# Kernel optimization log

Hardware: AMD Instinct MI355X
Metric: run time of the kernel (lower is better)

The kernel has to match this reference:

```python
import jax, jax.numpy as jnp
import numpy as np


def lstm_scan(x, W, U, b, hidden):
    """Keras-style LSTM. x: [B,T,D]. Returns full hidden sequence [B,T,H].
    Gate order i,f,c,o; sigmoid recurrent activation, tanh cell activation."""
    B, T, D = x.shape
    H = hidden
    # Precompute input projections for all timesteps in one big GEMM: [B,T,4H]
    xz = jnp.einsum('btd,dk->btk', x, W) + b
    xz = jnp.transpose(xz, (1, 0, 2))  # [T,B,4H] for scan

    def step(carry, xz_t):
        h, c = carry
        z = xz_t + h @ U  # [B,4H]
        i = jax.nn.sigmoid(z[:, 0*H:1*H])
        f = jax.nn.sigmoid(z[:, 1*H:2*H])
        g = jnp.tanh(z[:, 2*H:3*H])
        o = jax.nn.sigmoid(z[:, 3*H:4*H])
        c_new = f * c + i * g
        h_new = o * jnp.tanh(c_new)
        return (h_new, c_new), h_new

    h0 = jnp.zeros((B, H), dtype=x.dtype)
    c0 = jnp.zeros((B, H), dtype=x.dtype)
    _, hs = jax.lax.scan(step, (h0, c0), xz)  # hs: [T,B,H]
    return jnp.transpose(hs, (1, 0, 2))  # [B,T,H]


def setup_inputs() -> dict:
    key = jax.random.key(0)
    ks = jax.random.split(key, 9)
    B, T, D = 512, 512, 300
    H1, H2, C = 128, 32, 14
    s = lambda fan: 1.0 / np.sqrt(fan)
    return {
        'x':  jax.random.normal(ks[0], (B, T, D), dtype=jnp.float32),
        'W1': jax.random.normal(ks[1], (D, 4 * H1), dtype=jnp.float32) * s(D),
        'U1': jax.random.normal(ks[2], (H1, 4 * H1), dtype=jnp.float32) * s(H1),
        'b1': jnp.zeros((4 * H1,), dtype=jnp.float32),
        'W2': jax.random.normal(ks[3], (H1, 4 * H2), dtype=jnp.float32) * s(H1),
        'U2': jax.random.normal(ks[4], (H2, 4 * H2), dtype=jnp.float32) * s(H2),
        'b2': jnp.zeros((4 * H2,), dtype=jnp.float32),
        'Wd': jax.random.normal(ks[5], (H2, C), dtype=jnp.float32) * s(H2),
        'bd': jnp.zeros((C,), dtype=jnp.float32),
    }


def reference(x, W1, U1, b1, W2, U2, b2, Wd, bd):
    h1 = lstm_scan(x, W1, U1, b1, 128)      # [B,T,128] (return_sequences=True)
    h2 = lstm_scan(h1, W2, U2, b2, 32)      # [B,T,32]
    h2_last = h2[:, -1, :]                  # return_sequences=False -> last step
    return jax.nn.softmax(h2_last @ Wd + bd, axis=-1)  # [B,14]
```

## Files before the change

### kernel.cpp

```cpp
#include <hip/hip_runtime.h>
#include <math.h>

#define TC 128
#define NC 4
#define BATCH 512
#define T_TOTAL 512
#define D_IN 300
#define KP1 320
#define H1 128
#define G1 512
#define H2 32
#define NCLS 14

typedef unsigned short u16;
typedef __attribute__((ext_vector_type(8))) _Float16 f16x8;
typedef __attribute__((ext_vector_type(4))) float f32x4;

__device__ __forceinline__ float fexp2(float x) { return __builtin_amdgcn_exp2f(x); }
__device__ __forceinline__ float frcp(float x)  { return __builtin_amdgcn_rcpf(x); }
__device__ __forceinline__ float sig_f(float x) { return frcp(1.0f + fexp2(-1.44269504f * x)); }
__device__ __forceinline__ float th_f(float x)  { return 1.0f - 2.0f * frcp(1.0f + fexp2(2.88539008f * x)); }

__device__ __forceinline__ void lds_barrier() {
    asm volatile("s_waitcnt lgkmcnt(0)" ::: "memory");
    __builtin_amdgcn_s_barrier();
}

__global__ void prep_weights(const float* __restrict__ U1, _Float16* __restrict__ U1p,
                             const float* __restrict__ U2, _Float16* __restrict__ U2p,
                             const float* __restrict__ W1, _Float16* __restrict__ W1T,
                             const float* __restrict__ W2, _Float16* __restrict__ W2T,
                             const float* __restrict__ b1, float* __restrict__ b1p,
                             const float* __restrict__ b2, float* __restrict__ b2p)
{
    int idx = blockIdx.x * 256 + threadIdx.x;
    if (idx < 512 * 128) {
        int p = idx >> 7, k = idx & 127;
        int orig = ((p >> 4) & 3) * 128 + ((p >> 6) << 4) + (p & 15);
        U1p[p * 128 + k] = (_Float16)U1[k * 512 + orig];
    }
    if (idx < 512 * 320) {
        int p = idx / 320, k = idx % 320;
        int orig = ((p >> 4) & 3) * 128 + ((p >> 6) << 4) + (p & 15);
        W1T[p * 320 + k] = (_Float16)((k < D_IN) ? W1[k * 512 + orig] : 0.f);
    }
    if (idx < 128 * 128) {
        int p = idx >> 7, k = idx & 127;
        int orig = ((p >> 4) & 3) * 32 + ((p >> 6) << 4) + (p & 15);
        W2T[p * 128 + k] = (_Float16)W2[k * 128 + orig];
    }
    if (idx < 128 * 32) {
        int p = idx >> 5, k = idx & 31;
        int orig = ((p >> 4) & 3) * 32 + ((p >> 6) << 4) + (p & 15);
        U2p[p * 32 + k] = (_Float16)U2[k * 128 + orig];
    }
    if (idx < 512) {
        int orig = ((idx >> 4) & 3) * 128 + ((idx >> 6) << 4) + (idx & 15);
        b1p[idx] = b1[orig];
    }
    if (idx < 128) {
        int orig = ((idx >> 4) & 3) * 32 + ((idx >> 6) << 4) + (idx & 15);
        b2p[idx] = b2[orig];
    }
}

__global__ void xsplit(const float* __restrict__ x, _Float16* __restrict__ xh)
{
    long gid = (long)blockIdx.x * 256 + threadIdx.x;
    if (gid >= 262144L * 40) return;
    int m  = (int)(gid / 40);
    int s  = (int)(gid % 40);
    int k0 = s * 8;
    const float* xr = x + (long)m * D_IN + k0;
    float4 v0 = {0.f, 0.f, 0.f, 0.f}, v1 = {0.f, 0.f, 0.f, 0.f};
    if (s < 37) {
        v0 = *(const float4*)(xr);
        v1 = *(const float4*)(xr + 4);
    } else if (s == 37) {
        v0 = *(const float4*)(xr);
    }
    f16x8 o;
    o[0] = (_Float16)v0.x; o[1] = (_Float16)v0.y;
    o[2] = (_Float16)v0.z; o[3] = (_Float16)v0.w;
    o[4] = (_Float16)v1.x; o[5] = (_Float16)v1.y;
    o[6] = (_Float16)v1.z; o[7] = (_Float16)v1.w;
    *(f16x8*)(xh + (long)m * KP1 + k0) = o;
}

template<int NK, int NT, bool XMAP>
__device__ __forceinline__ void gemm_mblock(
    const _Float16* __restrict__ A, const _Float16* __restrict__ B,
    const float* __restrict__ bias, float* __restrict__ C,
    int m0, int chunk)
{
    const int Nc = NT * 128;
    const int tid = threadIdx.x;
    const int l = tid & 63, w = tid >> 6;
    const int wm = w >> 2, wn = w & 3;
    const int lr = l & 15, q = l >> 4;
    const int koff = q * 8;
    const int LDA = NK * 32;

    const _Float16* ap[4];
#pragma unroll
    for (int fi = 0; fi < 4; fi++) {
        int m = m0 + wm * 64 + fi * 16 + lr;
        long row = XMAP ? ((long)(m >> 7) * T_TOTAL + (long)chunk * TC + (m & (TC - 1)))
                        : (long)m;
        ap[fi] = A + row * LDA + koff;
    }
    const _Float16* bp[NT * 2];
    float bv[NT * 2];
#pragma unroll
    for (int fj = 0; fj < NT * 2; fj++) {
        int col = (fj >> 1) * 128 + wn * 32 + (fj & 1) * 16 + lr;
        bp[fj] = B + (long)col * LDA + koff;
        bv[fj] = bias[col];
    }

    f32x4 acc[4][NT * 2];
#pragma unroll
    for (int fi = 0; fi < 4; fi++)
#pragma unroll
        for (int fj = 0; fj < NT * 2; fj++)
            acc[fi][fj] = (f32x4){bv[fj], bv[fj], bv[fj], bv[fj]};

    f16x8 acur[4], anxt[4];
#pragma unroll
    for (int fi = 0; fi < 4; fi++)
        acur[fi] = *(const f16x8*)(ap[fi]);

#pragma unroll
    for (int ks = 0; ks < NK; ks++) {
        f16x8 bb[NT * 2];
#pragma unroll
        for (int fj = 0; fj < NT * 2; fj++)
            bb[fj] = *(const f16x8*)(bp[fj] + ks * 32);
        if (ks + 1 < NK) {
#pragma unroll
            for (int fi = 0; fi < 4; fi++)
                anxt[fi] = *(const f16x8*)(ap[fi] + (ks + 1) * 32);
        }
#pragma unroll
        for (int fi = 0; fi < 4; fi++)
#pragma unroll
            for (int fj = 0; fj < NT * 2; fj++)
                acc[fi][fj] = __builtin_amdgcn_mfma_f32_16x16x32_f16(acur[fi], bb[fj], acc[fi][fj], 0, 0, 0);
#pragma unroll
        for (int fi = 0; fi < 4; fi++)
            acur[fi] = anxt[fi];
    }

#pragma unroll
    for (int fi = 0; fi < 4; fi++) {
        int mrow = m0 + wm * 64 + fi * 16 + q * 4;
#pragma unroll
        for (int fj = 0; fj < NT * 2; fj++) {
            int col = (fj >> 1) * 128 + wn * 32 + (fj & 1) * 16 + lr;
#pragma unroll
            for (int rr = 0; rr < 4; rr++)
                C[(long)(mrow + rr) * Nc + col] = acc[fi][fj][rr];
        }
    }
}

#define L1_DECL(P) float P##00, P##01, P##02, P##03, P##10, P##11, P##12, P##13, \
                         P##20, P##21, P##22, P##23, P##30, P##31, P##32, P##33;

#define L1_LOAD(P, T)                                                             \
    P##00 = xz[xr0 + (long)(T) * 512 +  0]; P##01 = xz[xr1 + (long)(T) * 512 +  0]; \
    P##02 = xz[xr2 + (long)(T) * 512 +  0]; P##03 = xz[xr3 + (long)(T) * 512 +  0]; \
    P##10 = xz[xr0 + (long)(T) * 512 + 16]; P##11 = xz[xr1 + (long)(T) * 512 + 16]; \
    P##12 = xz[xr2 + (long)(T) * 512 + 16]; P##13 = xz[xr3 + (long)(T) * 512 + 16]; \
    P##20 = xz[xr0 + (long)(T) * 512 + 32]; P##21 = xz[xr1 + (long)(T) * 512 + 32]; \
    P##22 = xz[xr2 + (long)(T) * 512 + 32]; P##23 = xz[xr3 + (long)(T) * 512 + 32]; \
    P##30 = xz[xr0 + (long)(T) * 512 + 48]; P##31 = xz[xr1 + (long)(T) * 512 + 48]; \
    P##32 = xz[xr2 + (long)(T) * 512 + 48]; P##33 = xz[xr3 + (long)(T) * 512 + 48];

#define L1_STEP(T, PB, XC, XN)                                                    \
{                                                                                 \
    f16x8 ah0 = *(const f16x8*)&Ah[(PB) * 2048 + lr * 128 + (((q     ) ^ lr) << 3)]; \
    f16x8 ah1 = *(const f16x8*)&Ah[(PB) * 2048 + lr * 128 + (((q +  4) ^ lr) << 3)]; \
    f16x8 ah2 = *(const f16x8*)&Ah[(PB) * 2048 + lr * 128 + (((q +  8) ^ lr) << 3)]; \
    f16x8 ah3 = *(const f16x8*)&Ah[(PB) * 2048 + lr * 128 + (((q + 12) ^ lr) << 3)]; \
    if (valid && (T) + 1 < TC) { L1_LOAD(XN, (T) + 1) }                           \
    f32x4 a0 = (f32x4){XC##00, XC##01, XC##02, XC##03};                           \
    f32x4 a1 = (f32x4){XC##10, XC##11, XC##12, XC##13};                           \
    f32x4 a2 = (f32x4){XC##20, XC##21, XC##22, XC##23};                           \
    f32x4 a3 = (f32x4){XC##30, XC##31, XC##32, XC##33};                           \
    a0 = __builtin_amdgcn_mfma_f32_16x16x32_f16(ah0, uh00, a0, 0, 0, 0);          \
    a1 = __builtin_amdgcn_mfma_f32_16x16x32_f16(ah0, uh10, a1, 0, 0, 0);          \
    a2 = __builtin_amdgcn_mfma_f32_16x16x32_f16(ah0, uh20, a2, 0, 0, 0);          \
    a3 = __builtin_amdgcn_mfma_f32_16x16x32_f16(ah0, uh30, a3, 0, 0, 0);          \
    a0 = __builtin_amdgcn_mfma_f32_16x16x32_f16(ah1, uh01, a0, 0, 0, 0);          \
    a1 = __builtin_amdgcn_mfma_f32_16x16x32_f16(ah1, uh11, a1, 0, 0, 0);          \
    a2 = __builtin_amdgcn_mfma_f32_16x16x32_f16(ah1, uh21, a2, 0, 0, 0);          \
    a3 = __builtin_amdgcn_mfma_f32_16x16x32_f16(ah1, uh31, a3, 0, 0, 0);          \
    a0 = __builtin_amdgcn_mfma_f32_16x16x32_f16(ah2, uh02, a0, 0, 0, 0);          \
    a1 = __builtin_amdgcn_mfma_f32_16x16x32_f16(ah2, uh12, a1, 0, 0, 0);          \
    a2 = __builtin_amdgcn_mfma_f32_16x16x32_f16(ah2, uh22, a2, 0, 0, 0);          \
    a3 = __builtin_amdgcn_mfma_f32_16x16x32_f16(ah2, uh32, a3, 0, 0, 0);          \
    a0 = __builtin_amdgcn_mfma_f32_16x16x32_f16(ah3, uh03, a0, 0, 0, 0);          \
    a1 = __builtin_amdgcn_mfma_f32_16x16x32_f16(ah3, uh13, a1, 0, 0, 0);          \
    a2 = __builtin_amdgcn_mfma_f32_16x16x32_f16(ah3, uh23, a2, 0, 0, 0);          \
    a3 = __builtin_amdgcn_mfma_f32_16x16x32_f16(ah3, uh33, a3, 0, 0, 0);          \
    float e0 = __shfl_xor(a0[2], 32, 64), g0 = __shfl_xor(a0[3], 32, 64);         \
    float e1 = __shfl_xor(a1[2], 32, 64), g1 = __shfl_xor(a1[3], 32, 64);         \
    float e2 = __shfl_xor(a2[2], 32, 64), g2 = __shfl_xor(a2[3], 32, 64);         \
    float e3 = __shfl_xor(a3[2], 32, 64), g3 = __shfl_xor(a3[3], 32, 64);         \
    float zA0 = hi ? e0 : a0[0], zA1 = hi ? e1 : a1[0];                           \
    float zA2 = hi ? e2 : a2[0], zA3 = hi ? e3 : a3[0];                           \
    float zB0 = hi ? g0 : a0[1], zB1 = hi ? g1 : a1[1];                           \
    float zB2 = hi ? g2 : a2[1], zB3 = hi ? g3 : a3[1];                           \
    {                                                                             \
        float iv = sig_f(zA0), fv = sig_f(zA1), gv = th_f(zA2), ov = sig_f(zA3);  \
        cstA = fv * cstA + iv * gv;                                               \
        float hv = ov * th_f(cstA);                                               \
        _Float16 hh = (_Float16)hv;                                               \
        Ah[((PB) ^ 1) * 2048 + rwA * 128 + idxA] = hh;                            \
        h1f[((long)(b0 + rwA) * TC + (T)) * 128 + cn] = hh;                       \
        if ((T) == TC - 1) {                                                      \
            s1h[(long)(b0 + rwA) * 128 + cn] = hv;                                \
            s1c[(long)(b0 + rwA) * 128 + cn] = cstA;                              \
        }                                                                         \
    }                                                                             \
    {                                                                             \
        float iv = sig_f(zB0), fv = sig_f(zB1), gv = th_f(zB2), ov = sig_f(zB3);  \
        cstB = fv * cstB + iv * gv;                                               \
        float hv = ov * th_f(cstB);                                               \
        _Float16 hh = (_Float16)hv;                                               \
        Ah[((PB) ^ 1) * 2048 + rwB * 128 + idxB] = hh;                            \
        h1f[((long)(b0 + rwB) * TC + (T)) * 128 + cn] = hh;                       \
        if ((T) == TC - 1) {                                                      \
            s1h[(long)(b0 + rwB) * 128 + cn] = hv;                                \
            s1c[(long)(b0 + rwB) * 128 + cn] = cstB;                              \
        }                                                                         \
    }                                                                             \
    lds_barrier();                                                                \
}

static __device__ __forceinline__ void lstm1_role(
    const float* __restrict__ xz, const _Float16* __restrict__ U1p,
    _Float16* __restrict__ h1f, float* __restrict__ s1h, float* __restrict__ s1c,
    int first, char* smc)
{
    const int tid = threadIdx.x;
    const int l = tid & 63, w = tid >> 6;
    const int lr = l & 15, q = l >> 4;
    const int koff = q * 8;
    const int cn = w * 16 + lr;
    const int b0 = blockIdx.x * 8;
    const int p0 = w * 64 + lr;
    const int bq = b0 + q * 4;
    const bool valid = (q < 2);
    const bool hi = (q >= 2);
    const int rwA = (q & 1) * 4 + (q >> 1) * 2;
    const int rwB = rwA + 1;
    const int idxA = (((cn >> 3) ^ rwA) << 3) + (cn & 7);
    const int idxB = (((cn >> 3) ^ rwB) << 3) + (cn & 7);

    _Float16* Ah = (_Float16*)smc;

    const long xr0 = ((long)(bq + 0) * TC) * 512 + p0;
    const long xr1 = ((long)(bq + 1) * TC) * 512 + p0;
    const long xr2 = ((long)(bq + 2) * TC) * 512 + p0;
    const long xr3 = ((long)(bq + 3) * TC) * 512 + p0;

    const _Float16* ub = U1p + (long)(w * 64 + lr) * 128 + koff;
    f16x8 uh00 = *(const f16x8*)(ub +    0 * 128 +  0);
    f16x8 uh01 = *(const f16x8*)(ub +    0 * 128 + 32);
    f16x8 uh02 = *(const f16x8*)(ub +    0 * 128 + 64);
    f16x8 uh03 = *(const f16x8*)(ub +    0 * 128 + 96);
    f16x8 uh10 = *(const f16x8*)(ub +   16 * 128 +  0);
    f16x8 uh11 = *(const f16x8*)(ub +   16 * 128 + 32);
    f16x8 uh12 = *(const f16x8*)(ub +   16 * 128 + 64);
    f16x8 uh13 = *(const f16x8*)(ub +   16 * 128 + 96);
    f16x8 uh20 = *(const f16x8*)(ub +   32 * 128 +  0);
    f16x8 uh21 = *(const f16x8*)(ub +   32 * 128 + 32);
    f16x8 uh22 = *(const f16x8*)(ub +   32 * 128 + 64);
    f16x8 uh23 = *(const f16x8*)(ub +   32 * 128 + 96);
    f16x8 uh30 = *(const f16x8*)(ub +   48 * 128 +  0);
    f16x8 uh31 = *(const f16x8*)(ub +   48 * 128 + 32);
    f16x8 uh32 = *(const f16x8*)(ub +   48 * 128 + 64);
    f16x8 uh33 = *(const f16x8*)(ub +   48 * 128 + 96);

#pragma unroll
    for (int r = 0; r < 4; r++) {
        int rw = q * 4 + r;
        float h = 0.f;
        if (valid && !first) h = s1h[(long)(b0 + rw) * 128 + cn];
        int idx = (((cn >> 3) ^ rw) << 3) + (cn & 7);
        Ah[rw * 128 + idx] = valid ? (_Float16)h : (_Float16)0.f;
        if (!valid) Ah[2048 + rw * 128 + idx] = (_Float16)0.f;
    }
    float cstA = 0.f, cstB = 0.f;
    if (!first) {
        cstA = s1c[(long)(b0 + rwA) * 128 + cn];
        cstB = s1c[(long)(b0 + rwB) * 128 + cn];
    }
    lds_barrier();

    L1_DECL(xa) L1_DECL(xb)
    if (valid) { L1_LOAD(xa, 0) }

    for (int t = 0; t < TC; t += 2) {
        L1_STEP(t,     0, xa, xb)
        L1_STEP(t + 1, 1, xb, xa)
    }
}

#define L2_LOAD(P, T)                                                             \
    P##00 = xz2[yr0 + (long)(T) * 128 +  0]; P##01 = xz2[yr1 + (long)(T) * 128 +  0]; \
    P##02 = xz2[yr2 + (long)(T) * 128 +  0]; P##03 = xz2[yr3 + (long)(T) * 128 +  0]; \
    P##10 = xz2[yr0 + (long)(T) * 128 + 16]; P##11 = xz2[yr1 + (long)(T) * 128 + 16]; \
    P##12 = xz2[yr2 + (long)(T) * 128 + 16]; P##13 = xz2[yr3 + (long)(T) * 128 + 16]; \
    P##20 = xz2[yr0 + (long)(T) * 128 + 32]; P##21 = xz2[yr1 + (long)(T) * 128 + 32]; \
    P##22 = xz2[yr2 + (long)(T) * 128 + 32]; P##23 = xz2[yr3 + (long)(T) * 128 + 32]; \
    P##30 = xz2[yr0 + (long)(T) * 128 + 48]; P##31 = xz2[yr1 + (long)(T) * 128 + 48]; \
    P##32 = xz2[yr2 + (long)(T) * 128 + 48]; P##33 = xz2[yr3 + (long)(T) * 128 + 48];

#define L2_STEP(T, PB, XC, XN)                                                    \
{                                                                                 \
    if (act) {                                                                    \
        f16x8 ah = *(const f16x8*)&Ah[(PB) * 640 + lr * 40 + koff];               \
        if ((T) + 1 < TC) { L2_LOAD(XN, (T) + 1) }                                \
        f32x4 a0 = (f32x4){XC##00, XC##01, XC##02, XC##03};                       \
        f32x4 a1 = (f32x4){XC##10, XC##11, XC##12, XC##13};                       \
        f32x4 a2 = (f32x4){XC##20, XC##21, XC##22, XC##23};                       \
        f32x4 a3 = (f32x4){XC##30, XC##31, XC##32, XC##33};                       \
        a0 = __builtin_amdgcn_mfma_f32_16x16x32_f16(ah, uh0, a0, 0, 0, 0);        \
        a1 = __builtin_amdgcn_mfma_f32_16x16x32_f16(ah, uh1, a1, 0, 0, 0);        \
        a2 = __builtin_amdgcn_mfma_f32_16x16x32_f16(ah, uh2, a2, 0, 0, 0);        \
        a3 = __builtin_amdgcn_mfma_f32_16x16x32_f16(ah, uh3, a3, 0, 0, 0);        \
        _Pragma("unroll")                                                         \
        for (int r = 0; r < 4; r++) {                                             \
            float iv = sig_f(a0[r]);                                              \
            float fv = sig_f(a1[r]);                                              \
            float gv = th_f(a2[r]);                                               \
            float ov = sig_f(a3[r]);                                              \
            float cc = (r == 0) ? cst0 : (r == 1) ? cst1 : (r == 2) ? cst2 : cst3;\
            cc = fv * cc + iv * gv;                                               \
            float hv = ov * th_f(cc);                                             \
            if (r == 0) cst0 = cc; else if (r == 1) cst1 = cc;                    \
            else if (r == 2) cst2 = cc; else cst3 = cc;                           \
            int rw = (q << 2) + r;                                                \
            Ah[((PB) ^ 1) * 640 + rw * 40 + cn] = (_Float16)hv;                   \
            if ((T) == TC - 1) {                                                  \
                s2h[(long)(b0 + rw) * 32 + cn] = hv;                              \
                s2c[(long)(b0 + rw) * 32 + cn] = cc;                              \
            }                                                                     \
        }                                                                         \
    }                                                                             \
    lds_barrier();                                                                \
}

static __device__ __forceinline__ void lstm2_role(
    const float* __restrict__ xz2, const _Float16* __restrict__ U2p,
    float* __restrict__ s2h, float* __restrict__ s2c, int first, char* smc)
{
    const int tid = threadIdx.x;
    const int b0 = (blockIdx.x - 64) * 16;
    const bool act = tid < 128;
    const int l = tid & 63, w = (tid >> 6) & 1;
    const int lr = l & 15, q = l >> 4;
    const int koff = q * 8;
    const int cn = w * 16 + lr;
    const int p0 = w * 64 + lr;
    const int bq = b0 + q * 4;

    const long yr0 = ((long)(bq + 0) * TC) * 128 + p0;
    const long yr1 = ((long)(bq + 1) * TC) * 128 + p0;
    const long yr2 = ((long)(bq + 2) * TC) * 128 + p0;
    const long yr3 = ((long)(bq + 3) * TC) * 128 + p0;

    _Float16* Ah = (_Float16*)smc;

    f16x8 uh0 = {}, uh1 = {}, uh2 = {}, uh3 = {};
    float cst0 = 0.f, cst1 = 0.f, cst2 = 0.f, cst3 = 0.f;
    L1_DECL(xa) L1_DECL(xb)

    if (act) {
        const _Float16* ub = U2p + (long)(w * 64 + lr) * 32 + koff;
        uh0 = *(const f16x8*)(ub +  0 * 32);
        uh1 = *(const f16x8*)(ub + 16 * 32);
        uh2 = *(const f16x8*)(ub + 32 * 32);
        uh3 = *(const f16x8*)(ub + 48 * 32);
#pragma unroll
        for (int r = 0; r < 4; r++) {
            int rw = q * 4 + r;
            float h = 0.f, c = 0.f;
            if (!first) {
                h = s2h[(long)(b0 + rw) * 32 + cn];
                c = s2c[(long)(b0 + rw) * 32 + cn];
            }
            if (r == 0) cst0 = c; else if (r == 1) cst1 = c;
            else if (r == 2) cst2 = c; else cst3 = c;
            Ah[rw * 40 + cn] = (_Float16)h;
        }
        L2_LOAD(xa, 0)
    }
    lds_barrier();

    for (int t = 0; t < TC; t += 2) {
        L2_STEP(t,     0, xa, xb)
        L2_STEP(t + 1, 1, xb, xa)
    }
}

__global__ void
__attribute__((amdgpu_flat_work_group_size(512, 512)))
__attribute__((amdgpu_waves_per_eu(2, 2)))
mega(
    const _Float16* __restrict__ xh,
    const _Float16* __restrict__ W1T, const float* __restrict__ b1p,
    const _Float16* __restrict__ W2T, const float* __restrict__ b2p,
    const _Float16* __restrict__ U1p, const _Float16* __restrict__ U2p,
    float* xz1_0, float* xz1_1, float* xz2_0, float* xz2_1,
    _Float16* h1f_0, _Float16* h1f_1,
    float* s1h, float* s1c, float* s2h, float* s2c,
    int cA, int cB, int g1, int g2)
{
    __shared__ __align__(16) char sm[8192];
    int bid = blockIdx.x;

    if (cA >= 0 && bid < 64) {
        const float* xz = (cA & 1) ? xz1_1 : xz1_0;
        _Float16* hf = (cA & 1) ? h1f_1 : h1f_0;
        lstm1_role(xz, U1p, hf, s1h, s1c, cA == 0, sm);
        return;
    }
    if (cB >= 0 && bid >= 64 && bid < 96) {
        const float* xz2 = (cB & 1) ? xz2_1 : xz2_0;
        lstm2_role(xz2, U2p, s2h, s2c, cB == 0, sm);
        return;
    }
    int cwid = bid, ncw = 256;
    if (cA >= 0) { ncw -= 64; cwid -= 64; }
    if (cB >= 0) { ncw -= 32; if (bid >= 96) cwid -= 32; }
    int ng1 = (g1 >= 0) ? (BATCH * TC / 128) : 0;
    int ng2 = (g2 >= 0) ? (BATCH * TC / 128) : 0;
    float* xz1o = (g1 >= 0 && (g1 & 1)) ? xz1_1 : xz1_0;
    float* xz2o = (g2 >= 0 && (g2 & 1)) ? xz2_1 : xz2_0;
    const _Float16* hf = (g2 >= 0 && (g2 & 1)) ? h1f_1 : h1f_0;
    for (int it = cwid; it < ng1 + ng2; it += ncw) {
        if (it < ng1)
            gemm_mblock<10, 4, true>(xh, W1T, b1p, xz1o, it * 128, g1);
        else
            gemm_mblock<4, 1, false>(hf, W2T, b2p, xz2o, (it - ng1) * 128, 0);
    }
}

__global__ __launch_bounds__(256)
void head_kernel(const float* __restrict__ h2, const float* __restrict__ Wd,
                 const float* __restrict__ bd, float* __restrict__ out)
{
    int b = blockIdx.x * 256 + threadIdx.x;
    float h[H2];
#pragma unroll
    for (int k = 0; k < H2; k += 4)
        *(float4*)&h[k] = *(const float4*)&h2[b * H2 + k];

    float lg[NCLS];
#pragma unroll
    for (int c = 0; c < NCLS; c++) lg[c] = bd[c];
#pragma unroll
    for (int k = 0; k < H2; k++) {
        float hv = h[k];
#pragma unroll
        for (int c = 0; c < NCLS; c++)
            lg[c] += hv * Wd[k * NCLS + c];
    }
    float m = lg[0];
#pragma unroll
    for (int c = 1; c < NCLS; c++) m = fmaxf(m, lg[c]);
    float s = 0.f;
#pragma unroll
    for (int c = 0; c < NCLS; c++) { lg[c] = __expf(lg[c] - m); s += lg[c]; }
    float inv = __fdividef(1.0f, s);
#pragma unroll
    for (int c = 0; c < NCLS; c++) out[b * NCLS + c] = lg[c] * inv;
}

extern "C" void kernel_launch(void* const* d_in, const int* in_sizes, int n_in,
                              void* d_out, int out_size, void* d_ws, size_t ws_size,
                              hipStream_t stream)
{
    const float* x  = (const float*)d_in[0];
    const float* W1 = (const float*)d_in[1];
    const float* U1 = (const float*)d_in[2];
    const float* b1 = (const float*)d_in[3];
    const float* W2 = (const float*)d_in[4];
    const float* U2 = (const float*)d_in[5];
    const float* b2 = (const float*)d_in[6];
    const float* Wd = (const float*)d_in[7];
    const float* bd = (const float*)d_in[8];
    float* out = (float*)d_out;

    char* ws = (char*)d_ws;
    float* xz1[2]    = {(float*)(ws + 0L),         (float*)(ws + 134217728L)};
    _Float16* xh     = (_Float16*)(ws + 268435456L);
    _Float16* h1f[2] = {(_Float16*)(ws + 436207616L), (_Float16*)(ws + 452984832L)};
    float* xz2[2]    = {(float*)(ws + 469762048L), (float*)(ws + 503316480L)};
    float* s1h       = (float*)(ws + 536870912L);
    float* s1c       = (float*)(ws + 537133056L);
    float* s2h       = (float*)(ws + 537395200L);
    float* s2c       = (float*)(ws + 537460736L);
    _Float16* U1p    = (_Float16*)(ws + 537526272L);
    _Float16* U2p    = (_Float16*)(ws + 537657344L);
    _Float16* W1T    = (_Float16*)(ws + 537665536L);
    _Float16* W2T    = (_Float16*)(ws + 537993216L);
    float* b1p       = (float*)(ws + 538025984L);
    float* b2p       = (float*)(ws + 538028032L);

    prep_weights<<<640, 256, 0, stream>>>(U1, U1p, U2, U2p, W1, W1T, W2, W2T,
                                          b1, b1p, b2, b2p);
    xsplit<<<40960, 256, 0, stream>>>(x, xh);

#define MEGA(cA_, cB_, g1_, g2_) \
    mega<<<256, 512, 0, stream>>>(xh, W1T, b1p, W2T, b2p, U1p, U2p, \
        xz1[0], xz1[1], xz2[0], xz2[1], h1f[0], h1f[1], \
        s1h, s1c, s2h, s2c, cA_, cB_, g1_, g2_)

    MEGA(-1, -1, 0, -1);
    for (int c = 0; c < NC; c++)
        MEGA(c, (c >= 2) ? c - 2 : -1, (c + 1 < NC) ? c + 1 : -1, (c >= 1) ? c - 1 : -1);
    MEGA(-1, NC - 2, -1, NC - 1);
    MEGA(-1, NC - 1, -1, -1);
#undef MEGA

    head_kernel<<<2, 256, 0, stream>>>(s2h, Wd, bd, out);
}
```

Measured before the change: 966.4 us.

## Chunk fp16 input conversion into mega launches and split MFMA accumulator chains

The standalone full-tensor fp32-to-fp16 conversion of x is split per time chunk. Only chunk 0 is converted up front, and chunks 1-3 are converted by the GEMM worker blocks inside the first two mega launches, so the conversion overlaps the LSTM recurrence blocks. Separately, the layer-1 recurrent step splits each gate's 4-deep dependent MFMA chain into two independent accumulators that are summed afterward, shortening the serial latency per timestep. The accumulator split costs extra registers and vector adds, and the fused conversion lengthens the worker portion of the first launches.

```diff
diff --git a/kernel.cpp b/kernel.cpp
--- a/kernel.cpp
+++ b/kernel.cpp
@@ -64,14 +64,15 @@
     }
 }
 
-__global__ void xsplit(const float* __restrict__ x, _Float16* __restrict__ xh)
-{
-    long gid = (long)blockIdx.x * 256 + threadIdx.x;
-    if (gid >= 262144L * 40) return;
-    int m  = (int)(gid / 40);
-    int s  = (int)(gid % 40);
+__device__ __forceinline__ void xsplit_item(const float* __restrict__ x,
+                                            _Float16* __restrict__ xh,
+                                            int chunk, long i)
+{
+    int rr = (int)(i / 40), s = (int)(i % 40);
+    int b = rr >> 7, tt = rr & 127;
+    long m = (long)b * T_TOTAL + (long)chunk * TC + tt;
     int k0 = s * 8;
-    const float* xr = x + (long)m * D_IN + k0;
+    const float* xr = x + m * D_IN + k0;
     float4 v0 = {0.f, 0.f, 0.f, 0.f}, v1 = {0.f, 0.f, 0.f, 0.f};
     if (s < 37) {
         v0 = *(const float4*)(xr);
@@ -84,7 +85,23 @@
     o[2] = (_Float16)v0.z; o[3] = (_Float16)v0.w;
     o[4] = (_Float16)v1.x; o[5] = (_Float16)v1.y;
     o[6] = (_Float16)v1.z; o[7] = (_Float16)v1.w;
-    *(f16x8*)(xh + (long)m * KP1 + k0) = o;
+    *(f16x8*)(xh + m * KP1 + k0) = o;
+}
+
+__global__ void xsplit_chunk(const float* __restrict__ x, _Float16* __restrict__ xh, int chunk)
+{
+    long gid = (long)blockIdx.x * 256 + threadIdx.x;
+    if (gid >= 65536L * 40) return;
+    xsplit_item(x, xh, chunk, gid);
+}
+
+__device__ __forceinline__ void xsplit_role(const float* __restrict__ x,
+                                            _Float16* __restrict__ xh,
+                                            int chunk, int cwid, int ncw)
+{
+    const int tid = threadIdx.x;
+    for (long i = (long)cwid * 512 + tid; i < 65536L * 40; i += (long)ncw * 512)
+        xsplit_item(x, xh, chunk, i);
 }
 
 template<int NK, int NT, bool XMAP>
@@ -184,26 +201,29 @@
     f16x8 ah2 = *(const f16x8*)&Ah[(PB) * 2048 + lr * 128 + (((q +  8) ^ lr) << 3)]; \
     f16x8 ah3 = *(const f16x8*)&Ah[(PB) * 2048 + lr * 128 + (((q + 12) ^ lr) << 3)]; \
     if (valid && (T) + 1 < TC) { L1_LOAD(XN, (T) + 1) }                           \
-    f32x4 a0 = (f32x4){XC##00, XC##01, XC##02, XC##03};                           \
-    f32x4 a1 = (f32x4){XC##10, XC##11, XC##12, XC##13};                           \
-    f32x4 a2 = (f32x4){XC##20, XC##21, XC##22, XC##23};                           \
-    f32x4 a3 = (f32x4){XC##30, XC##31, XC##32, XC##33};                           \
-    a0 = __builtin_amdgcn_mfma_f32_16x16x32_f16(ah0, uh00, a0, 0, 0, 0);          \
-    a1 = __builtin_amdgcn_mfma_f32_16x16x32_f16(ah0, uh10, a1, 0, 0, 0);          \
-    a2 = __builtin_amdgcn_mfma_f32_16x16x32_f16(ah0, uh20, a2, 0, 0, 0);          \
-    a3 = __builtin_amdgcn_mfma_f32_16x16x32_f16(ah0, uh30, a3, 0, 0, 0);          \
-    a0 = __builtin_amdgcn_mfma_f32_16x16x32_f16(ah1, uh01, a0, 0, 0, 0);          \
-    a1 = __builtin_amdgcn_mfma_f32_16x16x32_f16(ah1, uh11, a1, 0, 0, 0);          \
-    a2 = __builtin_amdgcn_mfma_f32_16x16x32_f16(ah1, uh21, a2, 0, 0, 0);          \
-    a3 = __builtin_amdgcn_mfma_f32_16x16x32_f16(ah1, uh31, a3, 0, 0, 0);          \
-    a0 = __builtin_amdgcn_mfma_f32_16x16x32_f16(ah2, uh02, a0, 0, 0, 0);          \
-    a1 = __builtin_amdgcn_mfma_f32_16x16x32_f16(ah2, uh12, a1, 0, 0, 0);          \
-    a2 = __builtin_amdgcn_mfma_f32_16x16x32_f16(ah2, uh22, a2, 0, 0, 0);          \
-    a3 = __builtin_amdgcn_mfma_f32_16x16x32_f16(ah2, uh32, a3, 0, 0, 0);          \
-    a0 = __builtin_amdgcn_mfma_f32_16x16x32_f16(ah3, uh03, a0, 0, 0, 0);          \
-    a1 = __builtin_amdgcn_mfma_f32_16x16x32_f16(ah3, uh13, a1, 0, 0, 0);          \
-    a2 = __builtin_amdgcn_mfma_f32_16x16x32_f16(ah3, uh23, a2, 0, 0, 0);          \
-    a3 = __builtin_amdgcn_mfma_f32_16x16x32_f16(ah3, uh33, a3, 0, 0, 0);          \
+    f32x4 a0a = (f32x4){XC##00, XC##01, XC##02, XC##03};                          \
+    f32x4 a1a = (f32x4){XC##10, XC##11, XC##12, XC##13};                          \
+    f32x4 a2a = (f32x4){XC##20, XC##21, XC##22, XC##23};                          \
+    f32x4 a3a = (f32x4){XC##30, XC##31, XC##32, XC##33};                          \
+    f32x4 a0b = (f32x4){0.f, 0.f, 0.f, 0.f};                                      \
+    f32x4 a1b = a0b, a2b = a0b, a3b = a0b;                                        \
+    a0a = __builtin_amdgcn_mfma_f32_16x16x32_f16(ah0, uh00, a0a, 0, 0, 0);        \
+    a1a = __builtin_amdgcn_mfma_f32_16x16x32_f16(ah0, uh10, a1a, 0, 0, 0);        \
+    a2a = __builtin_amdgcn_mfma_f32_16x16x32_f16(ah0, uh20, a2a, 0, 0, 0);        \
+    a3a = __builtin_amdgcn_mfma_f32_16x16x32_f16(ah0, uh30, a3a, 0, 0, 0);        \
+    a0b = __builtin_amdgcn_mfma_f32_16x16x32_f16(ah1, uh01, a0b, 0, 0, 0);        \
+    a1b = __builtin_amdgcn_mfma_f32_16x16x32_f16(ah1, uh11, a1b, 0, 0, 0);        \
+    a2b = __builtin_amdgcn_mfma_f32_16x16x32_f16(ah1, uh21, a2b, 0, 0, 0);        \
+    a3b = __builtin_amdgcn_mfma_f32_16x16x32_f16(ah1, uh31, a3b, 0, 0, 0);        \
+    a0a = __builtin_amdgcn_mfma_f32_16x16x32_f16(ah2, uh02, a0a, 0, 0, 0);        \
+    a1a = __builtin_amdgcn_mfma_f32_16x16x32_f16(ah2, uh12, a1a, 0, 0, 0);        \
+    a2a = __builtin_amdgcn_mfma_f32_16x16x32_f16(ah2, uh22, a2a, 0, 0, 0);        \
+    a3a = __builtin_amdgcn_mfma_f32_16x16x32_f16(ah2, uh32, a3a, 0, 0, 0);        \
+    a0b = __builtin_amdgcn_mfma_f32_16x16x32_f16(ah3, uh03, a0b, 0, 0, 0);        \
+    a1b = __builtin_amdgcn_mfma_f32_16x16x32_f16(ah3, uh13, a1b, 0, 0, 0);        \
+    a2b = __builtin_amdgcn_mfma_f32_16x16x32_f16(ah3, uh23, a2b, 0, 0, 0);        \
+    a3b = __builtin_amdgcn_mfma_f32_16x16x32_f16(ah3, uh33, a3b, 0, 0, 0);        \
+    f32x4 a0 = a0a + a0b, a1 = a1a + a1b, a2 = a2a + a2b, a3 = a3a + a3b;         \
     float e0 = __shfl_xor(a0[2], 32, 64), g0 = __shfl_xor(a0[3], 32, 64);         \
     float e1 = __shfl_xor(a1[2], 32, 64), g1 = __shfl_xor(a1[3], 32, 64);         \
     float e2 = __shfl_xor(a2[2], 32, 64), g2 = __shfl_xor(a2[3], 32, 64);         \
@@ -411,14 +431,14 @@
 __attribute__((amdgpu_flat_work_group_size(512, 512)))
 __attribute__((amdgpu_waves_per_eu(2, 2)))
 mega(
-    const _Float16* __restrict__ xh,
+    const float* __restrict__ x, _Float16* __restrict__ xh,
     const _Float16* __restrict__ W1T, const float* __restrict__ b1p,
     const _Float16* __restrict__ W2T, const float* __restrict__ b2p,
     const _Float16* __restrict__ U1p, const _Float16* __restrict__ U2p,
     float* xz1_0, float* xz1_1, float* xz2_0, float* xz2_1,
     _Float16* h1f_0, _Float16* h1f_1,
     float* s1h, float* s1c, float* s2h, float* s2c,
-    int cA, int cB, int g1, int g2)
+    int cA, int cB, int g1, int g2, int xsA, int xsB)
 {
     __shared__ __align__(16) char sm[8192];
     int bid = blockIdx.x;
@@ -437,6 +457,8 @@
     int cwid = bid, ncw = 256;
     if (cA >= 0) { ncw -= 64; cwid -= 64; }
     if (cB >= 0) { ncw -= 32; if (bid >= 96) cwid -= 32; }
+    if (xsA >= 0) xsplit_role(x, xh, xsA, cwid, ncw);
+    if (xsB >= 0) xsplit_role(x, xh, xsB, cwid, ncw);
     int ng1 = (g1 >= 0) ? (BATCH * TC / 128) : 0;
     int ng2 = (g2 >= 0) ? (BATCH * TC / 128) : 0;
     float* xz1o = (g1 >= 0 && (g1 & 1)) ? xz1_1 : xz1_0;
@@ -514,18 +536,20 @@
 
     prep_weights<<<640, 256, 0, stream>>>(U1, U1p, U2, U2p, W1, W1T, W2, W2T,
                                           b1, b1p, b2, b2p);
-    xsplit<<<40960, 256, 0, stream>>>(x, xh);
-
-#define MEGA(cA_, cB_, g1_, g2_) \
-    mega<<<256, 512, 0, stream>>>(xh, W1T, b1p, W2T, b2p, U1p, U2p, \
+    xsplit_chunk<<<10240, 256, 0, stream>>>(x, xh, 0);
+
+#define MEGA(cA_, cB_, g1_, g2_, xsA_, xsB_) \
+    mega<<<256, 512, 0, stream>>>(x, xh, W1T, b1p, W2T, b2p, U1p, U2p, \
         xz1[0], xz1[1], xz2[0], xz2[1], h1f[0], h1f[1], \
-        s1h, s1c, s2h, s2c, cA_, cB_, g1_, g2_)
-
-    MEGA(-1, -1, 0, -1);
-    for (int c = 0; c < NC; c++)
-        MEGA(c, (c >= 2) ? c - 2 : -1, (c + 1 < NC) ? c + 1 : -1, (c >= 1) ? c - 1 : -1);
-    MEGA(-1, NC - 2, -1, NC - 1);
-    MEGA(-1, NC - 1, -1, -1);
+        s1h, s1c, s2h, s2c, cA_, cB_, g1_, g2_, xsA_, xsB_)
+
+    MEGA(-1, -1, 0, -1, 1, 2);
+    MEGA(0, -1, 1, -1, 3, -1);
+    MEGA(1, -1, 2, 0, -1, -1);
+    MEGA(2, 0, 3, 1, -1, -1);
+    MEGA(3, 1, -1, 2, -1, -1);
+    MEGA(-1, 2, -1, 3, -1, -1);
+    MEGA(-1, 3, -1, -1, -1, -1);
 #undef MEGA
 
     head_kernel<<<2, 256, 0, stream>>>(s2h, Wd, bd, out);
```

Measured after the change: 992.2 us. 1.03x slower.

## Split fp32-to-fp16 input conversion per chunk and overlap it inside mega launches

Applied to the files above, without the earlier changes.

The full-tensor xsplit pre-pass is replaced by a chunk-0-only conversion kernel. The conversion for chunks 1..3 now runs as a role inside the spare GEMM workgroups of earlier mega launches, so it can overlap the recurrent LSTM roles. This hides most of the conversion's memory traffic behind the serial recurrence. In exchange it adds work to the GEMM workers in those launches, which could lengthen them if they are on the critical path.

```diff
diff --git a/kernel.cpp b/kernel.cpp
--- a/kernel.cpp
+++ b/kernel.cpp
@@ -64,14 +64,15 @@
     }
 }
 
-__global__ void xsplit(const float* __restrict__ x, _Float16* __restrict__ xh)
-{
-    long gid = (long)blockIdx.x * 256 + threadIdx.x;
-    if (gid >= 262144L * 40) return;
-    int m  = (int)(gid / 40);
-    int s  = (int)(gid % 40);
+__device__ __forceinline__ void xsplit_item(const float* __restrict__ x,
+                                            _Float16* __restrict__ xh,
+                                            int chunk, long i)
+{
+    int rr = (int)(i / 40), s = (int)(i % 40);
+    int b = rr >> 7, tt = rr & 127;
+    long m = (long)b * T_TOTAL + (long)chunk * TC + tt;
     int k0 = s * 8;
-    const float* xr = x + (long)m * D_IN + k0;
+    const float* xr = x + m * D_IN + k0;
     float4 v0 = {0.f, 0.f, 0.f, 0.f}, v1 = {0.f, 0.f, 0.f, 0.f};
     if (s < 37) {
         v0 = *(const float4*)(xr);
@@ -84,7 +85,23 @@
     o[2] = (_Float16)v0.z; o[3] = (_Float16)v0.w;
     o[4] = (_Float16)v1.x; o[5] = (_Float16)v1.y;
     o[6] = (_Float16)v1.z; o[7] = (_Float16)v1.w;
-    *(f16x8*)(xh + (long)m * KP1 + k0) = o;
+    *(f16x8*)(xh + m * KP1 + k0) = o;
+}
+
+__global__ void xsplit_chunk(const float* __restrict__ x, _Float16* __restrict__ xh, int chunk)
+{
+    long gid = (long)blockIdx.x * 256 + threadIdx.x;
+    if (gid >= 65536L * 40) return;
+    xsplit_item(x, xh, chunk, gid);
+}
+
+__device__ __forceinline__ void xsplit_role(const float* __restrict__ x,
+                                            _Float16* __restrict__ xh,
+                                            int chunk, int cwid, int ncw)
+{
+    const int tid = threadIdx.x;
+    for (long i = (long)cwid * 512 + tid; i < 65536L * 40; i += (long)ncw * 512)
+        xsplit_item(x, xh, chunk, i);
 }
 
 template<int NK, int NT, bool XMAP>
@@ -411,14 +428,14 @@
 __attribute__((amdgpu_flat_work_group_size(512, 512)))
 __attribute__((amdgpu_waves_per_eu(2, 2)))
 mega(
-    const _Float16* __restrict__ xh,
+    const float* __restrict__ x, _Float16* __restrict__ xh,
     const _Float16* __restrict__ W1T, const float* __restrict__ b1p,
     const _Float16* __restrict__ W2T, const float* __restrict__ b2p,
     const _Float16* __restrict__ U1p, const _Float16* __restrict__ U2p,
     float* xz1_0, float* xz1_1, float* xz2_0, float* xz2_1,
     _Float16* h1f_0, _Float16* h1f_1,
     float* s1h, float* s1c, float* s2h, float* s2c,
-    int cA, int cB, int g1, int g2)
+    int cA, int cB, int g1, int g2, int xs)
 {
     __shared__ __align__(16) char sm[8192];
     int bid = blockIdx.x;
@@ -437,6 +454,7 @@
     int cwid = bid, ncw = 256;
     if (cA >= 0) { ncw -= 64; cwid -= 64; }
     if (cB >= 0) { ncw -= 32; if (bid >= 96) cwid -= 32; }
+    if (xs >= 0) xsplit_role(x, xh, xs, cwid, ncw);
     int ng1 = (g1 >= 0) ? (BATCH * TC / 128) : 0;
     int ng2 = (g2 >= 0) ? (BATCH * TC / 128) : 0;
     float* xz1o = (g1 >= 0 && (g1 & 1)) ? xz1_1 : xz1_0;
@@ -514,18 +532,20 @@
 
     prep_weights<<<640, 256, 0, stream>>>(U1, U1p, U2, U2p, W1, W1T, W2, W2T,
                                           b1, b1p, b2, b2p);
-    xsplit<<<40960, 256, 0, stream>>>(x, xh);
-
-#define MEGA(cA_, cB_, g1_, g2_) \
-    mega<<<256, 512, 0, stream>>>(xh, W1T, b1p, W2T, b2p, U1p, U2p, \
+    xsplit_chunk<<<10240, 256, 0, stream>>>(x, xh, 0);
+
+#define MEGA(cA_, cB_, g1_, g2_, xs_) \
+    mega<<<256, 512, 0, stream>>>(x, xh, W1T, b1p, W2T, b2p, U1p, U2p, \
         xz1[0], xz1[1], xz2[0], xz2[1], h1f[0], h1f[1], \
-        s1h, s1c, s2h, s2c, cA_, cB_, g1_, g2_)
-
-    MEGA(-1, -1, 0, -1);
-    for (int c = 0; c < NC; c++)
-        MEGA(c, (c >= 2) ? c - 2 : -1, (c + 1 < NC) ? c + 1 : -1, (c >= 1) ? c - 1 : -1);
-    MEGA(-1, NC - 2, -1, NC - 1);
-    MEGA(-1, NC - 1, -1, -1);
+        s1h, s1c, s2h, s2c, cA_, cB_, g1_, g2_, xs_)
+
+    MEGA(-1, -1, 0, -1, 1);
+    MEGA(0, -1, 1, -1, 2);
+    MEGA(1, -1, 2, 0, 3);
+    MEGA(2, 0, 3, 1, -1);
+    MEGA(3, 1, -1, 2, -1);
+    MEGA(-1, 2, -1, 3, -1);
+    MEGA(-1, 3, -1, -1, -1);
 #undef MEGA
 
     head_kernel<<<2, 256, 0, stream>>>(s2h, Wd, bd, out);
```

Measured after the change: 952.7 us. Within noise of the previous version (-1.4%).
